# Optimization experiments

Hardware: AMD Instinct MI355X
Metric: run time of the kernel (lower is better)

## Reference

```python
import jax, jax.numpy as jnp
import numpy as np
import itertools

B, N, C, D = 2, 150000, 64, 128  # samples, points/sample, channels, voxel grid extent
EPS = 1e-4  # BatchNormBlock eps
# 3x3x3 submanifold kernel offsets (27 taps)
OFFS = jnp.array(list(itertools.product((-1, 0, 1), repeat=3)), dtype=jnp.int32)  # [27,3]


def setup_inputs() -> dict:
    key = jax.random.key(0)
    k1, k2 = jax.random.split(key)
    rng = np.random.default_rng(0)
    # unique voxel coordinates per sample on a D^3 grid
    pos = np.stack([
        np.stack(np.unravel_index(rng.choice(D ** 3, size=N, replace=False), (D, D, D)), axis=-1)
        for _ in range(B)
    ]).astype(np.int32)  # [B,N,3]
    feats = jax.random.normal(k1, (B, N, C), jnp.float32)
    # 4 submanifold convs (2 residual blocks x 2 convs), fan-in scaled
    Ws = jax.random.normal(k2, (4, 27, C, C), jnp.float32) / np.sqrt(27 * C)
    gammas = jnp.ones((4, C), jnp.float32)
    betas = jnp.zeros((4, C), jnp.float32)
    return {"feats": feats, "Ws": Ws, "gammas": gammas, "betas": betas, "pos": jnp.asarray(pos)}


def _build_lut(pos_b):  # pos_b: [N,3] int32 -> dense hash grid [D^3] of point index or -1
    code = (pos_b[:, 0] * D + pos_b[:, 1]) * D + pos_b[:, 2]
    return jnp.full((D ** 3,), -1, jnp.int32).at[code].set(jnp.arange(N, dtype=jnp.int32))


def _subconv(x, lut_b, pos_b, W):
    # submanifold sparse conv: per kernel tap, gather neighbor features and GEMM
    # x:[N,C], lut_b:[D^3], pos_b:[N,3], W:[27,Cin,Cout]
    def step(acc, kw):
        d, Wk = kw
        npos = pos_b + d  # [N,3]
        valid = jnp.all((npos >= 0) & (npos < D), axis=-1)
        code = (npos[:, 0] * D + npos[:, 1]) * D + npos[:, 2]
        nidx = lut_b[jnp.where(valid, code, 0)]
        valid = valid & (nidx >= 0)
        g = jnp.where(valid[:, None], x[jnp.clip(nidx, 0, N - 1)], 0.0)  # [N,Cin]
        return acc + g @ Wk, None

    acc0 = jnp.zeros((x.shape[0], W.shape[-1]), x.dtype)
    acc, _ = jax.lax.scan(step, acc0, (OFFS, W))
    return acc


def _bn_relu(x, g, b):
    # BatchNormBlock (train mode, biased var over all concatenated points) + ReLU
    mu = x.mean(axis=(0, 1))
    var = jnp.mean(jnp.square(x - mu), axis=(0, 1))
    return jax.nn.relu((x - mu) * jax.lax.rsqrt(var + EPS) * g + b)


def reference(feats, Ws, gammas, betas, pos):
    lut = jax.vmap(_build_lut)(pos)  # [B, D^3]
    conv = jax.vmap(_subconv, in_axes=(0, 0, 0, None))
    x = feats
    for blk in range(2):  # conv_block_reps ResidualBlocks (NIN is Identity since nIn==nOut)
        out1 = x
        h = _bn_relu(x, gammas[2 * blk], betas[2 * blk])
        h = conv(h, lut, pos, Ws[2 * blk])
        h = _bn_relu(h, gammas[2 * blk + 1], betas[2 * blk + 1])
        out2 = conv(h, lut, pos, Ws[2 * blk + 1])
        x = out1 + out2
    return x
```

## Files before the change

### kernel.cpp

```cpp
#include <hip/hip_runtime.h>
#include <stdint.h>

#define DGRID 128
#define D3 (DGRID * DGRID * DGRID)
#define NBATCH 2
#define NPTS 150000
#define NROWS (NBATCH * NPTS)
#define NPAD 300032
#define ZROW NROWS
#define NCBLK (NPAD / 128)
#define NCELLS 8192
#define EPSBN 1e-4f

typedef __attribute__((ext_vector_type(8))) short s16x8;
typedef __attribute__((ext_vector_type(4))) float f32x4;

static __device__ __forceinline__ uint32_t f2bf_rne(float f) {
  uint32_t b = __float_as_uint(f);
  return (b + 0x7FFFu + ((b >> 16) & 1u)) >> 16;
}

static __device__ __forceinline__ uint32_t pkbf(float lo, float hi) {
  uint32_t r;
  asm("v_cvt_pk_bf16_f32 %0, %1, %2" : "=v"(r) : "v"(lo), "v"(hi));
  return r;
}

static __device__ __forceinline__ f32x4 mfma16(uint4 a, uint4 b, f32x4 c) {
  return __builtin_amdgcn_mfma_f32_16x16x32_bf16(
      __builtin_bit_cast(s16x8, a), __builtin_bit_cast(s16x8, b), c, 0, 0, 0);
}

static __device__ __forceinline__ uint4 bnrelu_frag(uint4 u, float4 aL, float4 aH,
                                                    float4 bL, float4 bH, bool vld) {
  float y0, y1;
  uint4 o;
  y0 = fmaxf(fmaf(__uint_as_float(u.x << 16), aL.x, bL.x), 0.f);
  y1 = fmaxf(fmaf(__uint_as_float(u.x & 0xFFFF0000u), aL.y, bL.y), 0.f);
  o.x = pkbf(y0, y1);
  y0 = fmaxf(fmaf(__uint_as_float(u.y << 16), aL.z, bL.z), 0.f);
  y1 = fmaxf(fmaf(__uint_as_float(u.y & 0xFFFF0000u), aL.w, bL.w), 0.f);
  o.y = pkbf(y0, y1);
  y0 = fmaxf(fmaf(__uint_as_float(u.z << 16), aH.x, bH.x), 0.f);
  y1 = fmaxf(fmaf(__uint_as_float(u.z & 0xFFFF0000u), aH.y, bH.y), 0.f);
  o.z = pkbf(y0, y1);
  y0 = fmaxf(fmaf(__uint_as_float(u.w << 16), aH.z, bH.z), 0.f);
  y1 = fmaxf(fmaf(__uint_as_float(u.w & 0xFFFF0000u), aH.w, bH.w), 0.f);
  o.w = pkbf(y0, y1);
  if (!vld) o = (uint4){0u, 0u, 0u, 0u};
  return o;
}

__global__ void k_scatter(const int* __restrict__ pos, int* __restrict__ lut) {
  int g = blockIdx.x * blockDim.x + threadIdx.x;
  if (g >= NROWS) return;
  int b = g / NPTS;
  int i = g - b * NPTS;
  lut[(size_t)b * D3 + (pos[3 * g] * DGRID + pos[3 * g + 1]) * DGRID + pos[3 * g + 2]] = i;
}

__global__ void k_cellcount(const int* __restrict__ pos, int* __restrict__ cnt) {
  int g = blockIdx.x * blockDim.x + threadIdx.x;
  if (g >= NROWS) return;
  int b = g / NPTS;
  int cid = (b << 12) | ((pos[3 * g] >> 3) << 8) | ((pos[3 * g + 1] >> 3) << 4) |
            (pos[3 * g + 2] >> 3);
  atomicAdd(&cnt[cid], 1);
}

__global__ void k_scan(const int* __restrict__ cnt, int* __restrict__ cstart) {
  __shared__ int s[1024];
  int tid = threadIdx.x;
  int e[8];
  int sum = 0;
#pragma unroll
  for (int j = 0; j < 8; j++) {
    int v = cnt[tid * 8 + j];
    e[j] = sum;
    sum += v;
  }
  s[tid] = sum;
  __syncthreads();
  for (int off = 1; off < 1024; off <<= 1) {
    int t = (tid >= off) ? s[tid - off] : 0;
    __syncthreads();
    s[tid] += t;
    __syncthreads();
  }
  int base = tid ? s[tid - 1] : 0;
#pragma unroll
  for (int j = 0; j < 8; j++) cstart[tid * 8 + j] = base + e[j];
}

__global__ void k_bucket(const int* __restrict__ pos, const int* __restrict__ cstart,
                         int* __restrict__ fill, int* __restrict__ perm,
                         int* __restrict__ iperm) {
  int g = blockIdx.x * blockDim.x + threadIdx.x;
  if (g >= NROWS) return;
  int b = g / NPTS;
  int cid = (b << 12) | ((pos[3 * g] >> 3) << 8) | ((pos[3 * g + 1] >> 3) << 4) |
            (pos[3 * g + 2] >> 3);
  int slot = cstart[cid] + atomicAdd(&fill[cid], 1);
  perm[slot] = g;
  iperm[g] = slot;
}

__global__ void k_nbr_s(const int* __restrict__ pos, const int* __restrict__ lut,
                        const int* __restrict__ perm, const int* __restrict__ iperm,
                        int* __restrict__ nbr) {
  int s = blockIdx.x * blockDim.x + threadIdx.x;
  if (s >= NPAD) return;
  if (s >= NROWS) {
#pragma unroll
    for (int t = 0; t < 27; ++t) nbr[(size_t)t * NPAD + s] = ZROW;
    return;
  }
  int g = perm[s];
  int b = g / NPTS;
  int x = pos[3 * g], y = pos[3 * g + 1], z = pos[3 * g + 2];
  const int* L = lut + (size_t)b * D3;
  const int* ip = iperm + (size_t)b * NPTS;
#pragma unroll
  for (int t = 0; t < 27; ++t) {
    int nx = x + t / 9 - 1;
    int ny = y + (t / 3) % 3 - 1;
    int nz = z + t % 3 - 1;
    int v = ZROW;
    if ((unsigned)nx < DGRID && (unsigned)ny < DGRID && (unsigned)nz < DGRID) {
      int n = L[(nx * DGRID + ny) * DGRID + nz];
      if (n >= 0) v = ip[n];
    }
    nbr[(size_t)t * NPAD + s] = v;
  }
}

__global__ void k_wpack(const float* __restrict__ Ws, uint4* __restrict__ Wfrag) {
  int e = blockIdx.x * 256 + threadIdx.x;
  if (e >= 4 * 27 * 512) return;
  int lane = e & 63, nb = (e >> 6) & 3, s = (e >> 8) & 1, tt = e >> 9;
  int kb = s * 32 + (lane >> 4) * 8;
  int cout = nb * 16 + (lane & 15);
  const float* src = Ws + (size_t)tt * 4096;
  uint32_t p[4];
#pragma unroll
  for (int j = 0; j < 4; ++j) {
    uint32_t lo = f2bf_rne(src[(kb + 2 * j) * 64 + cout]);
    uint32_t hi = f2bf_rne(src[(kb + 2 * j + 1) * 64 + cout]);
    p[j] = (hi << 16) | lo;
  }
  uint4 o;
  o.x = p[0]; o.y = p[1]; o.z = p[2]; o.w = p[3];
  Wfrag[e] = o;
}

__global__ void k_stats2(const float* __restrict__ part, int nblk,
                         const float* __restrict__ gamma, const float* __restrict__ beta,
                         float* __restrict__ chanp, int cid) {
  __shared__ float s[512];
  int c = threadIdx.x & 63, q = threadIdx.x >> 6;
  float sm = 0.f, sq = 0.f;
  for (int rb = q; rb < nblk; rb += 4) {
    sm += part[rb * 128 + c];
    sq += part[rb * 128 + 64 + c];
  }
  s[threadIdx.x] = sm;
  s[256 + threadIdx.x] = sq;
  __syncthreads();
  if (q == 0) {
    sm = s[c] + s[64 + c] + s[128 + c] + s[192 + c];
    sq = s[256 + c] + s[320 + c] + s[384 + c] + s[448 + c];
    float mean = sm / (float)NROWS;
    float var = sq / (float)NROWS - mean * mean;
    float a = gamma[cid * 64 + c] * rsqrtf(var + EPSBN);
    chanp[cid * 128 + c] = a;
    chanp[cid * 128 + 64 + c] = beta[cid * 64 + c] - mean * a;
  }
}

__global__ void k_cast(const float* __restrict__ feats, const int* __restrict__ perm,
                       uint4* __restrict__ f0, float* __restrict__ part) {
  __shared__ float sred[2][4][64];
  int tid = threadIdx.x, wv = tid >> 6, lane = tid & 63;
  int oct = tid & 7;
  float sm[8], sq[8];
#pragma unroll
  for (int j = 0; j < 8; j++) sm[j] = sq[j] = 0.f;
#pragma unroll 1
  for (int it = 0; it < 8; it++) {
    int g = blockIdx.x * 2048 + it * 256 + tid;
    int s = g >> 3;
    uint4 o = (uint4){0u, 0u, 0u, 0u};
    if (s < NROWS) {
      int src = perm[s];
      const float* X = feats + (size_t)src * 64 + oct * 8;
      float4 x0 = *(const float4*)X;
      float4 x1 = *(const float4*)(X + 4);
      sm[0] += x0.x; sq[0] += x0.x * x0.x;
      sm[1] += x0.y; sq[1] += x0.y * x0.y;
      sm[2] += x0.z; sq[2] += x0.z * x0.z;
      sm[3] += x0.w; sq[3] += x0.w * x0.w;
      sm[4] += x1.x; sq[4] += x1.x * x1.x;
      sm[5] += x1.y; sq[5] += x1.y * x1.y;
      sm[6] += x1.z; sq[6] += x1.z * x1.z;
      sm[7] += x1.w; sq[7] += x1.w * x1.w;
      o.x = pkbf(x0.x, x0.y);
      o.y = pkbf(x0.z, x0.w);
      o.z = pkbf(x1.x, x1.y);
      o.w = pkbf(x1.z, x1.w);
    }
    f0[g] = o;
  }
#pragma unroll
  for (int j = 0; j < 8; j++) {
    sm[j] += __shfl_xor(sm[j], 8);  sq[j] += __shfl_xor(sq[j], 8);
    sm[j] += __shfl_xor(sm[j], 16); sq[j] += __shfl_xor(sq[j], 16);
    sm[j] += __shfl_xor(sm[j], 32); sq[j] += __shfl_xor(sq[j], 32);
  }
  if (lane < 8) {
#pragma unroll
    for (int j = 0; j < 8; j++) {
      sred[0][wv][lane * 8 + j] = sm[j];
      sred[1][wv][lane * 8 + j] = sq[j];
    }
  }
  __syncthreads();
  if (tid < 64) {
    float s0 = 0.f, s1 = 0.f;
#pragma unroll
    for (int w = 0; w < 4; w++) {
      s0 += sred[0][w][tid];
      s1 += sred[1][w][tid];
    }
    part[blockIdx.x * 128 + tid] = s0;
    part[blockIdx.x * 128 + 64 + tid] = s1;
  }
}

#define PH(T, AC, VC, WC, NIC)                                              \
  {                                                                         \
    uint4 af[2][2];                                                         \
    _Pragma("unroll") for (int rt = 0; rt < 2; rt++) {                      \
      bool vld = (VC[rt] != ZROW);                                          \
      af[rt][0] = bnrelu_frag(AC[rt][0], paL[0], paH[0], pbL[0], pbH[0], vld); \
      af[rt][1] = bnrelu_frag(AC[rt][1], paL[1], paH[1], pbL[1], pbH[1], vld); \
    }                                                                       \
    _Pragma("unroll") for (int s = 0; s < 2; s++)                           \
      _Pragma("unroll") for (int rt = 0; rt < 2; rt++)                      \
        _Pragma("unroll") for (int nb = 0; nb < 4; nb++)                    \
          acc[rt][nb] = mfma16(af[rt][s], WC[s * 4 + nb], acc[rt][nb]);     \
    _Pragma("unroll") for (int rt = 0; rt < 2; rt++) {                      \
      const uint4* hp = src + (size_t)NIC[rt] * 8 + lkg;                    \
      VC[rt] = NIC[rt];                                                     \
      AC[rt][0] = hp[0];                                                    \
      AC[rt][1] = hp[4];                                                    \
    }                                                                       \
    {                                                                       \
      int tn = (T) + 4 <= 26 ? (T) + 4 : 26;                                \
      NIC[0] = nbp[(size_t)tn * NPAD];                                      \
      NIC[1] = nbp[(size_t)tn * NPAD + 16];                                 \
    }                                                                       \
    {                                                                       \
      int tw = (T) + 2 <= 26 ? (T) + 2 : 26;                                \
      const uint4* wp = Wf + (size_t)tw * 512 + lane;                       \
      _Pragma("unroll") for (int i = 0; i < 8; i++) WC[i] = wp[i * 64];     \
    }                                                                       \
  }

__global__ __launch_bounds__(256, 2) void k_conv(
    const uint4* __restrict__ src, const uint4* __restrict__ Wf,
    const int* __restrict__ nbr, const float* __restrict__ chanp, int cid,
    const uint4* __restrict__ resb, uint4* __restrict__ outb,
    float* __restrict__ outf, const int* __restrict__ operm,
    float* __restrict__ part, int do_stats) {
  __shared__ char smem[19456];
  int tid = threadIdx.x, wv = tid >> 6, lane = tid & 63;
  int bid = (int)blockIdx.x;
  int sbid = (bid & 7) * (NCBLK / 8) + (bid >> 3);
  int tbase = (sbid * 4 + wv) * 32;
  int lrow = lane & 15, lkg = lane >> 4;

  const float* cp = chanp + cid * 128;
  float4 paL[2], paH[2], pbL[2], pbH[2];
#pragma unroll
  for (int s = 0; s < 2; s++) {
    paL[s] = *(const float4*)(cp + s * 32 + lkg * 8);
    paH[s] = *(const float4*)(cp + s * 32 + lkg * 8 + 4);
    pbL[s] = *(const float4*)(cp + 64 + s * 32 + lkg * 8);
    pbH[s] = *(const float4*)(cp + 64 + s * 32 + lkg * 8 + 4);
  }

  f32x4 acc[2][4];
#pragma unroll
  for (int i = 0; i < 2; i++)
#pragma unroll
    for (int j = 0; j < 4; j++) acc[i][j] = (f32x4){0.f, 0.f, 0.f, 0.f};

  const int* nbp = nbr + tbase + lrow;
  int niE[2], niO[2], vE[2], vO[2];
  uint4 aE[2][2], aO[2][2], wE[8], wO[8];
  {
    int p0[2], p1[2];
    p0[0] = nbp[0];
    p0[1] = nbp[16];
    p1[0] = nbp[NPAD];
    p1[1] = nbp[NPAD + 16];
    niE[0] = nbp[(size_t)2 * NPAD];
    niE[1] = nbp[(size_t)2 * NPAD + 16];
    niO[0] = nbp[(size_t)3 * NPAD];
    niO[1] = nbp[(size_t)3 * NPAD + 16];
#pragma unroll
    for (int rt = 0; rt < 2; rt++) {
      const uint4* hp = src + (size_t)p0[rt] * 8 + lkg;
      aE[rt][0] = hp[0];
      aE[rt][1] = hp[4];
      vE[rt] = p0[rt];
    }
#pragma unroll
    for (int rt = 0; rt < 2; rt++) {
      const uint4* hp = src + (size_t)p1[rt] * 8 + lkg;
      aO[rt][0] = hp[0];
      aO[rt][1] = hp[4];
      vO[rt] = p1[rt];
    }
    const uint4* wp = Wf + lane;
#pragma unroll
    for (int i = 0; i < 8; i++) wE[i] = wp[i * 64];
    const uint4* wq = Wf + 512 + lane;
#pragma unroll
    for (int i = 0; i < 8; i++) wO[i] = wq[i * 64];
  }

#pragma unroll 1
  for (int t = 0; t < 26; t += 2) {
    PH(t, aE, vE, wE, niE)
    PH(t + 1, aO, vO, wO, niO)
  }
  PH(26, aE, vE, wE, niE)

  float sm4[4] = {0.f, 0.f, 0.f, 0.f}, sq4[4] = {0.f, 0.f, 0.f, 0.f};
  float* slab = (float*)smem + wv * 1088;
  float* sred = (float*)(smem + 17408);
#pragma unroll 1
  for (int rt = 0; rt < 2; rt++) {
#pragma unroll
    for (int nb = 0; nb < 4; nb++)
#pragma unroll
      for (int r = 0; r < 4; r++)
        slab[(lkg * 4 + r) * 68 + nb * 16 + lrow] = acc[rt][nb][r];
#pragma unroll
    for (int j = 0; j < 4; j++) {
      int row = tbase + rt * 16 + j * 4 + lkg;
      float4 vv = *(float4*)&slab[(j * 4 + lkg) * 68 + lrow * 4];
      bool live = row < NROWS;
      if (resb && live) {
        uint2 rb = *(const uint2*)((const char*)resb + (size_t)row * 128 + lrow * 8);
        vv.x += __uint_as_float(rb.x << 16);
        vv.y += __uint_as_float(rb.x & 0xFFFF0000u);
        vv.z += __uint_as_float(rb.y << 16);
        vv.w += __uint_as_float(rb.y & 0xFFFF0000u);
      }
      if (outb) {
        uint2 ob = (uint2){0u, 0u};
        if (live) {
          ob.x = pkbf(vv.x, vv.y);
          ob.y = pkbf(vv.z, vv.w);
        }
        *(uint2*)((char*)outb + (size_t)row * 128 + lrow * 8) = ob;
      }
      if (outf && live) {
        int orow = operm[row];
        *(float4*)(outf + (size_t)orow * 64 + lrow * 4) = vv;
      }
      if (live) {
        sm4[0] += vv.x; sq4[0] += vv.x * vv.x;
        sm4[1] += vv.y; sq4[1] += vv.y * vv.y;
        sm4[2] += vv.z; sq4[2] += vv.z * vv.z;
        sm4[3] += vv.w; sq4[3] += vv.w * vv.w;
      }
    }
  }
  if (do_stats) {
#pragma unroll
    for (int k = 0; k < 4; k++) {
      sm4[k] += __shfl_xor(sm4[k], 16); sq4[k] += __shfl_xor(sq4[k], 16);
      sm4[k] += __shfl_xor(sm4[k], 32); sq4[k] += __shfl_xor(sq4[k], 32);
    }
    if (lane < 16) {
#pragma unroll
      for (int k = 0; k < 4; k++) {
        sred[wv * 64 + lane * 4 + k] = sm4[k];
        sred[256 + wv * 64 + lane * 4 + k] = sq4[k];
      }
    }
    __syncthreads();
    if (tid < 64) {
      float s0 = 0.f, s1 = 0.f;
#pragma unroll
      for (int w = 0; w < 4; w++) {
        s0 += sred[w * 64 + tid];
        s1 += sred[256 + w * 64 + tid];
      }
      part[bid * 128 + tid] = s0;
      part[bid * 128 + 64 + tid] = s1;
    }
  }
}

extern "C" void kernel_launch(void* const* d_in, const int* in_sizes, int n_in,
                              void* d_out, int out_size, void* d_ws, size_t ws_size,
                              hipStream_t stream) {
  const float* feats = (const float*)d_in[0];
  const float* Ws = (const float*)d_in[1];
  const float* gammas = (const float*)d_in[2];
  const float* betas = (const float*)d_in[3];
  const int* pos = (const int*)d_in[4];
  float* out = (float*)d_out;

  char* w = (char*)d_ws;
  auto alloc = [&](size_t b) {
    char* p = w;
    w += (b + 255) & ~(size_t)255;
    return p;
  };
  int* nbr = (int*)alloc((size_t)27 * NPAD * 4);
  uint4* Wfrag = (uint4*)alloc((size_t)4 * 27 * 512 * 16);
  float* part = (float*)alloc((size_t)NCBLK * 128 * 4);
  float* chanp = (float*)alloc((size_t)4 * 128 * 4);
  int* perm = (int*)alloc((size_t)NPAD * 4);
  int* iperm = (int*)alloc((size_t)NROWS * 4);
  int* ccnt = (int*)alloc((size_t)NCELLS * 4);
  int* cfill = (int*)alloc((size_t)NCELLS * 4);
  int* cstart = (int*)alloc((size_t)NCELLS * 4);
  uint4* f0 = (uint4*)alloc((size_t)NPAD * 128);
  uint4* x1 = (uint4*)alloc((size_t)NPAD * 128);
  char* reg0 = alloc((size_t)NPAD * 128);
  uint4* c1 = (uint4*)reg0;
  int* lut = (int*)reg0;

  hipMemsetAsync(lut, 0xFF, (size_t)NBATCH * D3 * 4, stream);
  hipMemsetAsync(ccnt, 0, (size_t)NCELLS * 8, stream);
  int gpts = (NROWS + 255) / 256;
  k_scatter<<<gpts, 256, 0, stream>>>(pos, lut);
  k_cellcount<<<gpts, 256, 0, stream>>>(pos, ccnt);
  k_scan<<<1, 1024, 0, stream>>>(ccnt, cstart);
  k_bucket<<<gpts, 256, 0, stream>>>(pos, cstart, cfill, perm, iperm);
  k_nbr_s<<<NPAD / 256, 256, 0, stream>>>(pos, lut, perm, iperm, nbr);
  k_wpack<<<216, 256, 0, stream>>>(Ws, Wfrag);

  k_cast<<<1172, 256, 0, stream>>>(feats, perm, f0, part);
  k_stats2<<<1, 256, 0, stream>>>(part, 1172, gammas, betas, chanp, 0);

  k_conv<<<NCBLK, 256, 0, stream>>>(f0, Wfrag + 0 * 27 * 512, nbr, chanp, 0,
                                    nullptr, c1, nullptr, nullptr, part, 1);
  k_stats2<<<1, 256, 0, stream>>>(part, NCBLK, gammas, betas, chanp, 1);

  k_conv<<<NCBLK, 256, 0, stream>>>(c1, Wfrag + 1 * 27 * 512, nbr, chanp, 1,
                                    f0, x1, nullptr, nullptr, part, 1);
  k_stats2<<<1, 256, 0, stream>>>(part, NCBLK, gammas, betas, chanp, 2);

  k_conv<<<NCBLK, 256, 0, stream>>>(x1, Wfrag + 2 * 27 * 512, nbr, chanp, 2,
                                    nullptr, c1, nullptr, nullptr, part, 1);
  k_stats2<<<1, 256, 0, stream>>>(part, NCBLK, gammas, betas, chanp, 3);

  k_conv<<<NCBLK, 256, 0, stream>>>(c1, Wfrag + 3 * 27 * 512, nbr, chanp, 3,
                                    x1, nullptr, out, perm, part, 0);
}
```

Measured before the change: 1.285 ms.

## Precompute BN+ReLU activations in a separate pass instead of per-tap in conv

Adds a k_hb kernel that applies BN+ReLU once per row and writes a bf16 activation buffer, with padded and zero rows forced to zero. The conv kernel then gathers these ready activations and skips the per-tap normalisation that was repeated 27 times per row. Weight prefetch drops from two register sets to one (distance 1), and the min-occupancy hint is removed from launch bounds. This trades four extra elementwise passes over a ~38MB buffer for less VALU work and fewer registers inside the gather-GEMM loop, but the shorter weight prefetch distance may expose more load latency.

```diff
diff --git a/kernel.cpp b/kernel.cpp
--- a/kernel.cpp
+++ b/kernel.cpp
@@ -32,7 +32,7 @@
 }
 
 static __device__ __forceinline__ uint4 bnrelu_frag(uint4 u, float4 aL, float4 aH,
-                                                    float4 bL, float4 bH, bool vld) {
+                                                    float4 bL, float4 bH) {
   float y0, y1;
   uint4 o;
   y0 = fmaxf(fmaf(__uint_as_float(u.x << 16), aL.x, bL.x), 0.f);
@@ -47,7 +47,6 @@
   y0 = fmaxf(fmaf(__uint_as_float(u.w << 16), aH.z, bH.z), 0.f);
   y1 = fmaxf(fmaf(__uint_as_float(u.w & 0xFFFF0000u), aH.w, bH.w), 0.f);
   o.w = pkbf(y0, y1);
-  if (!vld) o = (uint4){0u, 0u, 0u, 0u};
   return o;
 }
 
@@ -236,21 +235,33 @@
   }
 }
 
-#define PH(T, AC, VC, WC, NIC)                                              \
+__global__ void k_hb(const uint4* __restrict__ x, const float* __restrict__ chanp,
+                     int cid, uint4* __restrict__ h) {
+  int tid = threadIdx.x;
+  int c0 = (tid & 7) * 8;
+  const float* cp = chanp + cid * 128;
+  float4 aL = *(const float4*)(cp + c0);
+  float4 aH = *(const float4*)(cp + c0 + 4);
+  float4 bL = *(const float4*)(cp + 64 + c0);
+  float4 bH = *(const float4*)(cp + 64 + c0 + 4);
+#pragma unroll 1
+  for (int it = 0; it < 8; it++) {
+    int g = blockIdx.x * 2048 + it * 256 + tid;
+    int row = g >> 3;
+    uint4 o = (uint4){0u, 0u, 0u, 0u};
+    if (row < NROWS) o = bnrelu_frag(x[g], aL, aH, bL, bH);
+    h[g] = o;
+  }
+}
+
+#define PH(T, AC, NIC)                                                      \
   {                                                                         \
-    uint4 af[2][2];                                                         \
-    _Pragma("unroll") for (int rt = 0; rt < 2; rt++) {                      \
-      bool vld = (VC[rt] != ZROW);                                          \
-      af[rt][0] = bnrelu_frag(AC[rt][0], paL[0], paH[0], pbL[0], pbH[0], vld); \
-      af[rt][1] = bnrelu_frag(AC[rt][1], paL[1], paH[1], pbL[1], pbH[1], vld); \
-    }                                                                       \
     _Pragma("unroll") for (int s = 0; s < 2; s++)                           \
       _Pragma("unroll") for (int rt = 0; rt < 2; rt++)                      \
         _Pragma("unroll") for (int nb = 0; nb < 4; nb++)                    \
-          acc[rt][nb] = mfma16(af[rt][s], WC[s * 4 + nb], acc[rt][nb]);     \
+          acc[rt][nb] = mfma16(AC[rt][s], wb[s * 4 + nb], acc[rt][nb]);     \
     _Pragma("unroll") for (int rt = 0; rt < 2; rt++) {                      \
       const uint4* hp = src + (size_t)NIC[rt] * 8 + lkg;                    \
-      VC[rt] = NIC[rt];                                                     \
       AC[rt][0] = hp[0];                                                    \
       AC[rt][1] = hp[4];                                                    \
     }                                                                       \
@@ -260,15 +271,15 @@
       NIC[1] = nbp[(size_t)tn * NPAD + 16];                                 \
     }                                                                       \
     {                                                                       \
-      int tw = (T) + 2 <= 26 ? (T) + 2 : 26;                                \
+      int tw = (T) + 1 <= 26 ? (T) + 1 : 26;                                \
       const uint4* wp = Wf + (size_t)tw * 512 + lane;                       \
-      _Pragma("unroll") for (int i = 0; i < 8; i++) WC[i] = wp[i * 64];     \
+      _Pragma("unroll") for (int i = 0; i < 8; i++) wb[i] = wp[i * 64];     \
     }                                                                       \
   }
 
-__global__ __launch_bounds__(256, 2) void k_conv(
+__global__ __launch_bounds__(256) void k_conv(
     const uint4* __restrict__ src, const uint4* __restrict__ Wf,
-    const int* __restrict__ nbr, const float* __restrict__ chanp, int cid,
+    const int* __restrict__ nbr,
     const uint4* __restrict__ resb, uint4* __restrict__ outb,
     float* __restrict__ outf, const int* __restrict__ operm,
     float* __restrict__ part, int do_stats) {
@@ -279,16 +290,6 @@
   int tbase = (sbid * 4 + wv) * 32;
   int lrow = lane & 15, lkg = lane >> 4;
 
-  const float* cp = chanp + cid * 128;
-  float4 paL[2], paH[2], pbL[2], pbH[2];
-#pragma unroll
-  for (int s = 0; s < 2; s++) {
-    paL[s] = *(const float4*)(cp + s * 32 + lkg * 8);
-    paH[s] = *(const float4*)(cp + s * 32 + lkg * 8 + 4);
-    pbL[s] = *(const float4*)(cp + 64 + s * 32 + lkg * 8);
-    pbH[s] = *(const float4*)(cp + 64 + s * 32 + lkg * 8 + 4);
-  }
-
   f32x4 acc[2][4];
 #pragma unroll
   for (int i = 0; i < 2; i++)
@@ -296,8 +297,8 @@
     for (int j = 0; j < 4; j++) acc[i][j] = (f32x4){0.f, 0.f, 0.f, 0.f};
 
   const int* nbp = nbr + tbase + lrow;
-  int niE[2], niO[2], vE[2], vO[2];
-  uint4 aE[2][2], aO[2][2], wE[8], wO[8];
+  int niE[2], niO[2];
+  uint4 aE[2][2], aO[2][2], wb[8];
   {
     int p0[2], p1[2];
     p0[0] = nbp[0];
@@ -313,29 +314,24 @@
       const uint4* hp = src + (size_t)p0[rt] * 8 + lkg;
       aE[rt][0] = hp[0];
       aE[rt][1] = hp[4];
-      vE[rt] = p0[rt];
     }
 #pragma unroll
     for (int rt = 0; rt < 2; rt++) {
       const uint4* hp = src + (size_t)p1[rt] * 8 + lkg;
       aO[rt][0] = hp[0];
       aO[rt][1] = hp[4];
-      vO[rt] = p1[rt];
     }
     const uint4* wp = Wf + lane;
 #pragma unroll
-    for (int i = 0; i < 8; i++) wE[i] = wp[i * 64];
-    const uint4* wq = Wf + 512 + lane;
-#pragma unroll
-    for (int i = 0; i < 8; i++) wO[i] = wq[i * 64];
+    for (int i = 0; i < 8; i++) wb[i] = wp[i * 64];
   }
 
 #pragma unroll 1
   for (int t = 0; t < 26; t += 2) {
-    PH(t, aE, vE, wE, niE)
-    PH(t + 1, aO, vO, wO, niO)
-  }
-  PH(26, aE, vE, wE, niE)
+    PH(t, aE, niE)
+    PH(t + 1, aO, niO)
+  }
+  PH(26, aE, niE)
 
   float sm4[4] = {0.f, 0.f, 0.f, 0.f}, sq4[4] = {0.f, 0.f, 0.f, 0.f};
   float* slab = (float*)smem + wv * 1088;
@@ -433,6 +429,7 @@
   int* cstart = (int*)alloc((size_t)NCELLS * 4);
   uint4* f0 = (uint4*)alloc((size_t)NPAD * 128);
   uint4* x1 = (uint4*)alloc((size_t)NPAD * 128);
+  uint4* h = (uint4*)alloc((size_t)NPAD * 128);
   char* reg0 = alloc((size_t)NPAD * 128);
   uint4* c1 = (uint4*)reg0;
   int* lut = (int*)reg0;
@@ -449,19 +446,22 @@
 
   k_cast<<<1172, 256, 0, stream>>>(feats, perm, f0, part);
   k_stats2<<<1, 256, 0, stream>>>(part, 1172, gammas, betas, chanp, 0);
-
-  k_conv<<<NCBLK, 256, 0, stream>>>(f0, Wfrag + 0 * 27 * 512, nbr, chanp, 0,
+  k_hb<<<1172, 256, 0, stream>>>(f0, chanp, 0, h);
+  k_conv<<<NCBLK, 256, 0, stream>>>(h, Wfrag + 0 * 27 * 512, nbr,
                                     nullptr, c1, nullptr, nullptr, part, 1);
+
   k_stats2<<<1, 256, 0, stream>>>(part, NCBLK, gammas, betas, chanp, 1);
-
-  k_conv<<<NCBLK, 256, 0, stream>>>(c1, Wfrag + 1 * 27 * 512, nbr, chanp, 1,
+  k_hb<<<1172, 256, 0, stream>>>(c1, chanp, 1, h);
+  k_conv<<<NCBLK, 256, 0, stream>>>(h, Wfrag + 1 * 27 * 512, nbr,
                                     f0, x1, nullptr, nullptr, part, 1);
+
   k_stats2<<<1, 256, 0, stream>>>(part, NCBLK, gammas, betas, chanp, 2);
-
-  k_conv<<<NCBLK, 256, 0, stream>>>(x1, Wfrag + 2 * 27 * 512, nbr, chanp, 2,
+  k_hb<<<1172, 256, 0, stream>>>(x1, chanp, 2, h);
+  k_conv<<<NCBLK, 256, 0, stream>>>(h, Wfrag + 2 * 27 * 512, nbr,
                                     nullptr, c1, nullptr, nullptr, part, 1);
+
   k_stats2<<<1, 256, 0, stream>>>(part, NCBLK, gammas, betas, chanp, 3);
-
-  k_conv<<<NCBLK, 256, 0, stream>>>(c1, Wfrag + 3 * 27 * 512, nbr, chanp, 3,
+  k_hb<<<1172, 256, 0, stream>>>(c1, chanp, 3, h);
+  k_conv<<<NCBLK, 256, 0, stream>>>(h, Wfrag + 3 * 27 * 512, nbr,
                                     x1, nullptr, out, perm, part, 0);
 }
```

New measurement: 1.234 ms. 4.0% less time.
